# Performance work log

Measured on AMD Instinct MI355X. Metric: run time of the kernel, lower is better.

The kernel has to match this reference:

```python
import jax, jax.numpy as jnp
import numpy as np

DIM = 1024
HEADS = 16
HEAD_DIM = DIM // HEADS
EPS = 1e-5


def layer_norm(x, w, b):
    # normalize over last dim (head_dim)
    mu = jnp.mean(x, axis=-1, keepdims=True)
    var = jnp.mean(jnp.square(x - mu), axis=-1, keepdims=True)
    return (x - mu) * jax.lax.rsqrt(var + EPS) * w + b


def setup_inputs() -> dict:
    key = jax.random.key(0)
    ks = jax.random.split(key, 8)
    B, N = 2, 2048
    x = jax.random.normal(ks[0], (B, N, DIM), dtype=jnp.float32)
    mask = jax.random.randint(ks[1], (B, 1, N, N), 0, 2) == 1  # True = masked out
    qkv_w = jax.random.normal(ks[2], (3 * DIM, DIM), dtype=jnp.float32) * (DIM ** -0.5)
    q_norm_w = jnp.ones((HEAD_DIM,), dtype=jnp.float32)
    q_norm_b = jnp.zeros((HEAD_DIM,), dtype=jnp.float32)
    k_norm_w = jnp.ones((HEAD_DIM,), dtype=jnp.float32)
    k_norm_b = jnp.zeros((HEAD_DIM,), dtype=jnp.float32)
    proj_w = jax.random.normal(ks[3], (DIM, DIM), dtype=jnp.float32) * (DIM ** -0.5)
    proj_b = jnp.zeros((DIM,), dtype=jnp.float32)
    return {"x": x, "mask": mask, "qkv_w": qkv_w,
            "q_norm_w": q_norm_w, "q_norm_b": q_norm_b,
            "k_norm_w": k_norm_w, "k_norm_b": k_norm_b,
            "proj_w": proj_w, "proj_b": proj_b}


def reference(x, mask, qkv_w, q_norm_w, q_norm_b, k_norm_w, k_norm_b, proj_w, proj_b):
    B, N, C = x.shape
    H, D = HEADS, HEAD_DIM
    scale = D ** -0.5
    # qkv projection (no bias), split into q,k,v of shape (B,H,N,D)
    qkv = (x @ qkv_w.T).reshape(B, N, 3, H, D).transpose(2, 0, 3, 1, 4)
    q, k, v = qkv[0], qkv[1], qkv[2]
    q = layer_norm(q, q_norm_w, q_norm_b)
    k = layer_norm(k, k_norm_w, k_norm_b)
    q = q * scale
    attn = jnp.einsum("bhnd,bhmd->bhnm", q, k)  # (B,H,N,N)
    attn = jnp.where(mask, -jnp.inf, attn)
    attn = jax.nn.softmax(attn, axis=-1)
    out = jnp.einsum("bhnm,bhmd->bhnd", attn, v)
    out = out.transpose(0, 2, 1, 3).reshape(B, N, C)
    return out @ proj_w.T + proj_b
```

## Files before the change

kernel.cpp:

```cpp
#include <hip/hip_runtime.h>
#include <hip/hip_bf16.h>
#include <math.h>

#define B_    2
#define N_    2048
#define DIM_  1024
#define H_    16
#define HD_   64
#define EPS_  1e-5f
#define SCALE_ 0.125f
#define LOG2E_ 1.4426950408889634f
#define MFIX_  14.0f

typedef __attribute__((ext_vector_type(8))) __bf16 bf16x8;
typedef __attribute__((ext_vector_type(8))) unsigned short ushort8;
typedef __attribute__((ext_vector_type(4))) float f32x4;
typedef __attribute__((ext_vector_type(4))) unsigned int uint4v;

__device__ __forceinline__ unsigned short f2bf(float x) {
    unsigned u = __builtin_bit_cast(unsigned, x);
    u += 0x7fff + ((u >> 16) & 1);
    return (unsigned short)(u >> 16);
}
__device__ __forceinline__ unsigned pk2bf(float a, float b) {
    unsigned ua = __builtin_bit_cast(unsigned, a) + 0x8000u;
    unsigned ub = __builtin_bit_cast(unsigned, b) + 0x8000u;
    return __builtin_amdgcn_perm(ub, ua, 0x07060302);
}
__device__ __forceinline__ unsigned cvtpk(float a, float b) {
    unsigned r;
    asm("v_cvt_pk_bf16_f32 %0, %1, %2" : "=v"(r) : "v"(a), "v"(b));
    return r;
}

__device__ __forceinline__ void gl_lds16(const void* g, void* l) {
    __builtin_amdgcn_global_load_lds(
        (const __attribute__((address_space(1))) void*)g,
        (__attribute__((address_space(3))) void*)l, 16, 0, 0);
}

__global__ __launch_bounds__(256) void cast_all_bf16(
    const float* __restrict__ x, const float* __restrict__ qkvw,
    const float* __restrict__ pw, unsigned short* __restrict__ out) {
    int i = (blockIdx.x * 256 + threadIdx.x) * 8;
    const float* src;
    if (i < 4194304) src = x + i;
    else if (i < 7340032) src = qkvw + (i - 4194304);
    else src = pw + (i - 7340032);
    float4 v0 = *(const float4*)src;
    float4 v1 = *(const float4*)(src + 4);
    ushort8 r;
    r[0] = f2bf(v0.x); r[1] = f2bf(v0.y); r[2] = f2bf(v0.z); r[3] = f2bf(v0.w);
    r[4] = f2bf(v1.x); r[5] = f2bf(v1.y); r[6] = f2bf(v1.z); r[7] = f2bf(v1.w);
    *(ushort8*)(out + i) = r;
}

__global__ __launch_bounds__(256) void pack_mask(
    const int* __restrict__ mask, unsigned long long* __restrict__ bm) {
    int w = blockIdx.x * 4 + (threadIdx.x >> 6);
    int lane = threadIdx.x & 63;
    int mv = mask[(size_t)w * 64 + lane];
    unsigned long long bits = __ballot(mv != 0);
    if (lane == 0) bm[w] = bits;
}

__global__ __launch_bounds__(256) void gemm_qkv_ln(
    const unsigned short* __restrict__ A, const unsigned short* __restrict__ Bw,
    const float* __restrict__ qnw, const float* __restrict__ qnb,
    const float* __restrict__ knw, const float* __restrict__ knb,
    unsigned short* __restrict__ qbuf, unsigned short* __restrict__ kbuf,
    unsigned short* __restrict__ vt) {
    const int K = DIM_;
    __shared__ unsigned short As[128 * 32];
    __shared__ unsigned short Bs[128 * 32];
    const int tid = threadIdx.x;
    const int wave = tid >> 6, lane = tid & 63;
    const int quad = lane >> 4, lcol = lane & 15;
    const int wr = wave >> 1, wc = wave & 1;
    const int row0 = blockIdx.y * 128, col0 = blockIdx.x * 128;

    f32x4 acc[4][4];
#pragma unroll
    for (int i = 0; i < 4; ++i)
#pragma unroll
        for (int j = 0; j < 4; ++j) acc[i][j] = (f32x4){0.f, 0.f, 0.f, 0.f};

    for (int k0 = 0; k0 < K; k0 += 32) {
        __syncthreads();
#pragma unroll
        for (int c = 0; c < 2; ++c) {
            int base = wave * 2048 + c * 1024;
            int myofs = base + lane * 16;
            int r = myofs >> 6;
            int kb = myofs & 63;
            gl_lds16((const char*)A + ((size_t)(row0 + r) * K + k0) * 2 + kb,
                     (char*)As + base);
            gl_lds16((const char*)Bw + ((size_t)(col0 + r) * K + k0) * 2 + kb,
                     (char*)Bs + base);
        }
        __syncthreads();

        bf16x8 af[4], bfr[4];
#pragma unroll
        for (int i = 0; i < 4; ++i) {
            af[i] = *(const bf16x8*)&As[(wr * 64 + i * 16 + lcol) * 32 + quad * 8];
            bfr[i] = *(const bf16x8*)&Bs[(wc * 64 + i * 16 + lcol) * 32 + quad * 8];
        }
#pragma unroll
        for (int i = 0; i < 4; ++i)
#pragma unroll
            for (int j = 0; j < 4; ++j)
                acc[i][j] = __builtin_amdgcn_mfma_f32_16x16x32_bf16(
                    af[i], bfr[j], acc[i][j], 0, 0, 0);
    }

    const int colbase = col0 + wc * 64;
    const int t = colbase >> 10;
    const int h = (colbase & 1023) >> 6;

    if (t < 2) {
        const float* wv = (t == 0) ? qnw : knw;
        const float* bv = (t == 0) ? qnb : knb;
        float wreg[4], breg[4];
#pragma unroll
        for (int j = 0; j < 4; ++j) {
            wreg[j] = wv[j * 16 + lcol];
            breg[j] = bv[j * 16 + lcol];
        }
        const float sc = (t == 0) ? (SCALE_ * LOG2E_) : 1.f;
        unsigned short* obase = (t == 0) ? qbuf : kbuf;
#pragma unroll
        for (int i = 0; i < 4; ++i) {
#pragma unroll
            for (int reg = 0; reg < 4; ++reg) {
                int row = row0 + wr * 64 + i * 16 + quad * 4 + reg;
                int bb = row >> 11, n = row & (N_ - 1);
                float v[4];
#pragma unroll
                for (int j = 0; j < 4; ++j) v[j] = acc[i][j][reg];
                float s = v[0] + v[1] + v[2] + v[3];
                s += __shfl_xor(s, 1);
                s += __shfl_xor(s, 2);
                s += __shfl_xor(s, 4);
                s += __shfl_xor(s, 8);
                float mu = s * (1.f / 64.f);
                float d[4], s2 = 0.f;
#pragma unroll
                for (int j = 0; j < 4; ++j) {
                    d[j] = v[j] - mu;
                    s2 += d[j] * d[j];
                }
                s2 += __shfl_xor(s2, 1);
                s2 += __shfl_xor(s2, 2);
                s2 += __shfl_xor(s2, 4);
                s2 += __shfl_xor(s2, 8);
                float r = rsqrtf(s2 * (1.f / 64.f) + EPS_);
                float o0 = (d[0] * r * wreg[0] + breg[0]) * sc;
                float o1 = (d[1] * r * wreg[1] + breg[1]) * sc;
                float o2 = (d[2] * r * wreg[2] + breg[2]) * sc;
                float o3 = (d[3] * r * wreg[3] + breg[3]) * sc;
                uint2 pk;
                pk.x = pk2bf(o0, o1);
                pk.y = pk2bf(o2, o3);
                *(uint2*)(obase + ((size_t)(bb * H_ + h) * N_ + n) * 64 +
                          lcol * 4) = pk;
            }
        }
    } else {
        const int rowb = row0 + wr * 64;
        const int bb = rowb >> 11;
        unsigned short* vtb =
            vt + ((size_t)(bb * H_ + h) * 64) * (size_t)N_ + (rowb & (N_ - 1));
#pragma unroll
        for (int i = 0; i < 4; ++i) {
            const int pos = (i >> 1) * 32 + quad * 8 + (i & 1) * 4;
#pragma unroll
            for (int jj = 0; jj < 4; ++jj) {
                uint2 pk;
                pk.x = pk2bf(acc[i][jj][0], acc[i][jj][1]);
                pk.y = pk2bf(acc[i][jj][2], acc[i][jj][3]);
                *(uint2*)(vtb + (size_t)(lcol + 16 * jj) * N_ + pos) = pk;
            }
        }
    }
}

__global__ __launch_bounds__(256) void gemm_proj(
    const unsigned short* __restrict__ A, const unsigned short* __restrict__ Bw,
    const float* __restrict__ bias, float* __restrict__ Cout) {
    const int K = DIM_;
    __shared__ unsigned short As[128 * 32];
    __shared__ unsigned short Bs[64 * 32];
    const int tid = threadIdx.x;
    const int wave = tid >> 6, lane = tid & 63;
    const int quad = lane >> 4, lcol = lane & 15;
    const int row0 = blockIdx.y * 128, col0 = blockIdx.x * 64;

    f32x4 acc[2][4];
#pragma unroll
    for (int i = 0; i < 2; ++i)
#pragma unroll
        for (int j = 0; j < 4; ++j) acc[i][j] = (f32x4){0.f, 0.f, 0.f, 0.f};

    for (int k0 = 0; k0 < K; k0 += 32) {
        __syncthreads();
#pragma unroll
        for (int pi = 0; pi < 3; ++pi) {
            int p = wave * 3 + pi;
            if (p < 8) {
                int base = p * 1024;
                int myofs = base + lane * 16;
                int r = myofs >> 6, kb = myofs & 63;
                gl_lds16((const char*)A + ((size_t)(row0 + r) * K + k0) * 2 + kb,
                         (char*)As + base);
            } else {
                int base = (p - 8) * 1024;
                int myofs = base + lane * 16;
                int r = myofs >> 6, kb = myofs & 63;
                gl_lds16((const char*)Bw + ((size_t)(col0 + r) * K + k0) * 2 + kb,
                         (char*)Bs + base);
            }
        }
        __syncthreads();

        bf16x8 af[2], bfr[4];
#pragma unroll
        for (int i = 0; i < 2; ++i)
            af[i] = *(const bf16x8*)&As[(wave * 32 + i * 16 + lcol) * 32 + quad * 8];
#pragma unroll
        for (int j = 0; j < 4; ++j)
            bfr[j] = *(const bf16x8*)&Bs[(j * 16 + lcol) * 32 + quad * 8];
#pragma unroll
        for (int i = 0; i < 2; ++i)
#pragma unroll
            for (int j = 0; j < 4; ++j)
                acc[i][j] = __builtin_amdgcn_mfma_f32_16x16x32_bf16(
                    af[i], bfr[j], acc[i][j], 0, 0, 0);
    }

#pragma unroll
    for (int i = 0; i < 2; ++i) {
#pragma unroll
        for (int j = 0; j < 4; ++j) {
            int col = col0 + j * 16 + lcol;
            float bv = bias[col];
#pragma unroll
            for (int reg = 0; reg < 4; ++reg) {
                int row = row0 + wave * 32 + i * 16 + quad * 4 + reg;
                Cout[(size_t)row * DIM_ + col] = acc[i][j][reg] + bv;
            }
        }
    }
}

#define WAITBAR(Ncnt)                                                     \
    asm volatile("s_waitcnt vmcnt(" #Ncnt ")" ::: "memory");              \
    __builtin_amdgcn_s_barrier();                                         \
    __builtin_amdgcn_sched_barrier(0);

#define ISSUE2(B0, B1)                                                    \
    {                                                                     \
        gl_lds16(kp0, (char*)Ks[B0] + kld0);                              \
        gl_lds16(kp1, (char*)Ks[B0] + kld1);                              \
        gl_lds16(vp0, (char*)Vts[B0] + kld0);                             \
        gl_lds16(vp1, (char*)Vts[B0] + kld1);                             \
        gl_lds16(kp0 + 8192, (char*)Ks[B1] + kld0);                       \
        gl_lds16(kp1 + 8192, (char*)Ks[B1] + kld1);                       \
        gl_lds16(vp0 + 128, (char*)Vts[B1] + kld0);                       \
        gl_lds16(vp1 + 128, (char*)Vts[B1] + kld1);                       \
        mm0[B0] = bmq0[0]; mm1[B0] = bmq1[0];                             \
        mm0[B1] = bmq0[1]; mm1[B1] = bmq1[1];                             \
        kp0 += 16384; kp1 += 16384; vp0 += 256; vp1 += 256;               \
        bmq0 += 2; bmq1 += 2;                                             \
    }

#define QKT(J, SACC, MWA, MWB)                                            \
    {                                                                     \
        unsigned long long mqa = (MWA) >> (quad * 4);                     \
        unsigned long long mqb = (MWB) >> (quad * 4);                     \
        unsigned ml[2][2];                                                \
        ml[0][0] = (unsigned)mqa; ml[0][1] = (unsigned)(mqa >> 32);       \
        ml[1][0] = (unsigned)mqb; ml[1][1] = (unsigned)(mqb >> 32);       \
        _Pragma("unroll")                                                 \
        for (int qf = 0; qf < 2; ++qf)                                    \
            _Pragma("unroll")                                             \
            for (int kt = 0; kt < 4; ++kt) {                              \
                unsigned word = ml[qf][kt >> 1];                          \
                _Pragma("unroll")                                         \
                for (int reg = 0; reg < 4; ++reg) {                       \
                    unsigned msk = (unsigned)(((int)(word <<              \
                        (31 - ((kt & 1) * 16 + reg)))) >> 31);            \
                    SACC[qf][kt][reg] = __builtin_bit_cast(float,         \
                        (msk & 0xc61c4000u) | (~msk & 0xc1600000u));      \
                }                                                         \
            }                                                             \
        __builtin_amdgcn_s_setprio(1);                                    \
        _Pragma("unroll")                                                 \
        for (int kt = 0; kt < 4; ++kt)                                    \
            _Pragma("unroll")                                             \
            for (int d0 = 0; d0 < 2; ++d0) {                              \
                bf16x8 ak = *(const bf16x8*)((const char*)Ks[J] +         \
                    (d0 * 4 + quad) * 1024 + kt * 256 + lofs);            \
                SACC[0][kt] = __builtin_amdgcn_mfma_f32_16x16x32_bf16(    \
                    ak, bq[0][d0], SACC[0][kt], 0, 0, 0);                 \
                SACC[1][kt] = __builtin_amdgcn_mfma_f32_16x16x32_bf16(    \
                    ak, bq[1][d0], SACC[1][kt], 0, 0, 0);                 \
            }                                                             \
        __builtin_amdgcn_s_setprio(0);                                    \
    }

#define SM(SACC, PK)                                                      \
    _Pragma("unroll")                                                     \
    for (int qf = 0; qf < 2; ++qf)                                        \
        _Pragma("unroll")                                                 \
        for (int kt = 0; kt < 4; ++kt) {                                  \
            float p0 = exp2f(SACC[qf][kt][0]);                            \
            float p1 = exp2f(SACC[qf][kt][1]);                            \
            float p2 = exp2f(SACC[qf][kt][2]);                            \
            float p3 = exp2f(SACC[qf][kt][3]);                            \
            PK[qf][kt].x = cvtpk(p0, p1);                                 \
            PK[qf][kt].y = cvtpk(p2, p3);                                 \
        }

#define PV(J, PK)                                                         \
    {                                                                     \
        __builtin_amdgcn_s_setprio(1);                                    \
        _Pragma("unroll")                                                 \
        for (int P = 0; P < 2; ++P) {                                     \
            bf16x8 bp[2];                                                 \
            _Pragma("unroll")                                             \
            for (int qf = 0; qf < 2; ++qf) {                              \
                uint4v bu;                                                \
                bu[0] = PK[qf][2 * P].x;  bu[1] = PK[qf][2 * P].y;        \
                bu[2] = PK[qf][2 * P + 1].x; bu[3] = PK[qf][2 * P + 1].y; \
                bp[qf] = __builtin_bit_cast(bf16x8, bu);                  \
                lacc[qf] = __builtin_amdgcn_mfma_f32_16x16x32_bf16(       \
                    ones, bp[qf], lacc[qf], 0, 0, 0);                     \
            }                                                             \
            _Pragma("unroll")                                             \
            for (int dt = 0; dt < 4; ++dt) {                              \
                bf16x8 va = *(const bf16x8*)((const char*)Vts[J] +        \
                    (P * 4 + quad) * 1024 + dt * 256 + lofs);             \
                oacc[0][dt] = __builtin_amdgcn_mfma_f32_16x16x32_bf16(    \
                    va, bp[0], oacc[0][dt], 0, 0, 0);                     \
                oacc[1][dt] = __builtin_amdgcn_mfma_f32_16x16x32_bf16(    \
                    va, bp[1], oacc[1][dt], 0, 0, 0);                     \
            }                                                             \
        }                                                                 \
        __builtin_amdgcn_s_setprio(0);                                    \
    }

#define PAIR(J0, J1)                                                      \
    {                                                                     \
        f32x4 saccA[2][4], saccB[2][4];                                   \
        uint2 pkA[2][4], pkB[2][4];                                       \
        QKT(J0, saccA, mm0[J0], mm1[J0])                                  \
        SM(saccA, pkA)                                                    \
        QKT(J1, saccB, mm0[J1], mm1[J1])                                  \
        PV(J0, pkA)                                                       \
        SM(saccB, pkB)                                                    \
        PV(J1, pkB)                                                       \
    }

__global__ __launch_bounds__(256, 2) void flash_attn_mfma9(
    const unsigned short* __restrict__ q, const unsigned short* __restrict__ k,
    const unsigned short* __restrict__ vt,
    const unsigned long long* __restrict__ bm, unsigned short* __restrict__ ao) {
    __shared__ unsigned short Qs[128 * 64];
    __shared__ unsigned short Ks[4][64 * 64];
    __shared__ unsigned short Vts[4][64 * 64];

    const int tid = threadIdx.x;
    const int wave = tid >> 6, lane = tid & 63;
    const int quad = lane >> 4, lcol = lane & 15;
    const int bh = blockIdx.y, b = bh >> 4, h = bh & 15;
    const int q0 = blockIdx.x * 128;
    const int lofs = (lcol ^ (quad * 2)) << 4;

    const char* kgbase = (const char*)k + (size_t)bh * N_ * 128;
    const char* vtbase = (const char*)vt + (size_t)bh * 64 * N_ * 2;

    const int c0 = wave * 2, c1 = c0 + 1;
    const int swz0 = (c0 & 3) * 2, swz1 = (c1 & 3) * 2;
    const int kld0 = c0 * 1024, kld1 = c1 * 1024;
    const char* kp0 = kgbase + (lane ^ swz0) * 128 + c0 * 16;
    const char* kp1 = kgbase + (lane ^ swz1) * 128 + c1 * 16;
    const char* vp0 = vtbase + (size_t)(lane ^ swz0) * (N_ * 2) + c0 * 16;
    const char* vp1 = vtbase + (size_t)(lane ^ swz1) * (N_ * 2) + c1 * 16;

    const unsigned long long* bmq0 =
        bm + ((size_t)b * N_ + q0 + wave * 32 + lcol) * 32;
    const unsigned long long* bmq1 = bmq0 + 16 * 32;
    unsigned long long mm0[4], mm1[4];

    {
        const char* qg = (const char*)(q + (size_t)(bh * N_ + q0) * 64);
#pragma unroll
        for (int c = 0; c < 4; ++c) {
            int base = wave * 4096 + c * 1024;
            gl_lds16(qg + base + lane * 16, (char*)Qs + base);
        }
    }
    asm volatile("" ::: "memory");
    __builtin_amdgcn_sched_barrier(0);
#pragma unroll
    for (int t = 0; t < 4; ++t) {
        gl_lds16(kp0, (char*)Ks[t] + kld0);
        gl_lds16(kp1, (char*)Ks[t] + kld1);
        gl_lds16(vp0, (char*)Vts[t] + kld0);
        gl_lds16(vp1, (char*)Vts[t] + kld1);
        mm0[t] = bmq0[t];
        mm1[t] = bmq1[t];
        kp0 += 8192; kp1 += 8192; vp0 += 128; vp1 += 128;
        __builtin_amdgcn_sched_barrier(0);
    }
    bmq0 += 4; bmq1 += 4;
    asm volatile("s_waitcnt vmcnt(24)" ::: "memory");
    __builtin_amdgcn_sched_barrier(0);

    bf16x8 bq[2][2];
#pragma unroll
    for (int qf = 0; qf < 2; ++qf)
#pragma unroll
        for (int d0 = 0; d0 < 2; ++d0)
            bq[qf][d0] = *(const bf16x8*)&Qs[(wave * 32 + qf * 16 + lcol) * 64 +
                                             d0 * 32 + quad * 8];

    ushort8 ot;
#pragma unroll
    for (int i = 0; i < 8; ++i) ot[i] = 0x3F80;
    const bf16x8 ones = __builtin_bit_cast(bf16x8, ot);

    f32x4 oacc[2][4];
#pragma unroll
    for (int qf = 0; qf < 2; ++qf)
#pragma unroll
        for (int dt = 0; dt < 4; ++dt) oacc[qf][dt] = (f32x4){0.f, 0.f, 0.f, 0.f};
    f32x4 lacc[2];
    lacc[0] = (f32x4){0.f, 0.f, 0.f, 0.f};
    lacc[1] = (f32x4){0.f, 0.f, 0.f, 0.f};

    WAITBAR(12)
    PAIR(0, 1)
    for (int g = 0; g < 7; ++g) {
        WAITBAR(0)
        ISSUE2(0, 1)
        PAIR(2, 3)
        WAITBAR(0)
        ISSUE2(2, 3)
        PAIR(0, 1)
    }
    WAITBAR(0)
    PAIR(2, 3)

#pragma unroll
    for (int qf = 0; qf < 2; ++qf) {
        float inv = 1.f / lacc[qf][0];
        int row = q0 + wave * 32 + qf * 16 + lcol;
        unsigned short* dst =
            ao + ((size_t)(b * N_ + row)) * DIM_ + h * 64 + quad * 4;
#pragma unroll
        for (int dt = 0; dt < 4; ++dt) {
            uint2 pko;
            pko.x = pk2bf(oacc[qf][dt][0] * inv, oacc[qf][dt][1] * inv);
            pko.y = pk2bf(oacc[qf][dt][2] * inv, oacc[qf][dt][3] * inv);
            *(uint2*)(dst + dt * 16) = pko;
        }
    }
}

extern "C" void kernel_launch(void* const* d_in, const int* in_sizes, int n_in,
                              void* d_out, int out_size, void* d_ws,
                              size_t ws_size, hipStream_t stream) {
    const float* x     = (const float*)d_in[0];
    const int*   mask  = (const int*)d_in[1];
    const float* qkv_w = (const float*)d_in[2];
    const float* qnw   = (const float*)d_in[3];
    const float* qnb   = (const float*)d_in[4];
    const float* knw   = (const float*)d_in[5];
    const float* knb   = (const float*)d_in[6];
    const float* pw    = (const float*)d_in[7];
    const float* pb    = (const float*)d_in[8];
    float* out = (float*)d_out;

    char* ws = (char*)d_ws;
    unsigned short* x_bf  = (unsigned short*)(ws + 0);
    unsigned short* qw_bf = (unsigned short*)(ws + 8388608);
    unsigned short* pw_bf = (unsigned short*)(ws + 14680064);
    unsigned short* qbuf  = (unsigned short*)(ws + 16777216);
    unsigned short* kbuf  = (unsigned short*)(ws + 25165824);
    unsigned short* ao_bnc= (unsigned short*)(ws + 33554432);
    unsigned short* vt    = (unsigned short*)(ws + 41943040);
    unsigned long long* bmask = (unsigned long long*)(ws + 50331648);

    cast_all_bf16<<<8388608 / 2048, 256, 0, stream>>>(x, qkv_w, pw, x_bf);

    pack_mask<<<(B_ * N_ * (N_ / 64)) / 4, 256, 0, stream>>>(mask, bmask);

    gemm_qkv_ln<<<dim3(3072 / 128, 4096 / 128), 256, 0, stream>>>(
        x_bf, qw_bf, qnw, qnb, knw, knb, qbuf, kbuf, vt);

    flash_attn_mfma9<<<dim3(N_ / 128, B_ * H_), 256, 0, stream>>>(
        qbuf, kbuf, vt, bmask, ao_bnc);

    gemm_proj<<<dim3(DIM_ / 64, 4096 / 128), 256, 0, stream>>>(
        ao_bnc, pw_bf, pb, out);
}
```

Before: 267.6 us.

## Double query rows per wave in flash attention to reuse K/V tiles

Each wave now processes 64 query rows (four 16-row fragments) instead of 32, so the block covers 256 queries and the grid halves. Every K and V tile loaded into shared memory is reused across twice as many queries, which cuts global K/V traffic and LDS reads per MFMA. In exchange, register pressure roughly doubles for the accumulators, so launch bounds drop to one block per SM. The grid becomes 8x32=256 blocks, which lowers occupancy and may underfill the device's compute units.

```diff
diff --git a/kernel.cpp b/kernel.cpp
--- a/kernel.cpp
+++ b/kernel.cpp
@@ -268,24 +268,24 @@
         gl_lds16(kp1 + 8192, (char*)Ks[B1] + kld1);                       \
         gl_lds16(vp0 + 128, (char*)Vts[B1] + kld0);                       \
         gl_lds16(vp1 + 128, (char*)Vts[B1] + kld1);                       \
-        mm0[B0] = bmq0[0]; mm1[B0] = bmq1[0];                             \
-        mm0[B1] = bmq0[1]; mm1[B1] = bmq1[1];                             \
+        _Pragma("unroll")                                                 \
+        for (int qf = 0; qf < 4; ++qf) {                                  \
+            mm[B0][qf] = bmq[qf][0];                                      \
+            mm[B1][qf] = bmq[qf][1];                                      \
+            bmq[qf] += 2;                                                 \
+        }                                                                 \
         kp0 += 16384; kp1 += 16384; vp0 += 256; vp1 += 256;               \
-        bmq0 += 2; bmq1 += 2;                                             \
-    }
-
-#define QKT(J, SACC, MWA, MWB)                                            \
+    }
+
+#define QKT(J, SACC, MROW)                                                \
     {                                                                     \
-        unsigned long long mqa = (MWA) >> (quad * 4);                     \
-        unsigned long long mqb = (MWB) >> (quad * 4);                     \
-        unsigned ml[2][2];                                                \
-        ml[0][0] = (unsigned)mqa; ml[0][1] = (unsigned)(mqa >> 32);       \
-        ml[1][0] = (unsigned)mqb; ml[1][1] = (unsigned)(mqb >> 32);       \
         _Pragma("unroll")                                                 \
-        for (int qf = 0; qf < 2; ++qf)                                    \
+        for (int qf = 0; qf < 4; ++qf) {                                  \
+            unsigned long long mq = (MROW)[qf] >> (quad * 4);             \
+            unsigned mlo = (unsigned)mq, mhi = (unsigned)(mq >> 32);      \
             _Pragma("unroll")                                             \
             for (int kt = 0; kt < 4; ++kt) {                              \
-                unsigned word = ml[qf][kt >> 1];                          \
+                unsigned word = (kt < 2) ? mlo : mhi;                     \
                 _Pragma("unroll")                                         \
                 for (int reg = 0; reg < 4; ++reg) {                       \
                     unsigned msk = (unsigned)(((int)(word <<              \
@@ -294,6 +294,7 @@
                         (msk & 0xc61c4000u) | (~msk & 0xc1600000u));      \
                 }                                                         \
             }                                                             \
+        }                                                                 \
         __builtin_amdgcn_s_setprio(1);                                    \
         _Pragma("unroll")                                                 \
         for (int kt = 0; kt < 4; ++kt)                                    \
@@ -301,17 +302,17 @@
             for (int d0 = 0; d0 < 2; ++d0) {                              \
                 bf16x8 ak = *(const bf16x8*)((const char*)Ks[J] +         \
                     (d0 * 4 + quad) * 1024 + kt * 256 + lofs);            \
-                SACC[0][kt] = __builtin_amdgcn_mfma_f32_16x16x32_bf16(    \
-                    ak, bq[0][d0], SACC[0][kt], 0, 0, 0);                 \
-                SACC[1][kt] = __builtin_amdgcn_mfma_f32_16x16x32_bf16(    \
-                    ak, bq[1][d0], SACC[1][kt], 0, 0, 0);                 \
+                _Pragma("unroll")                                         \
+                for (int qf = 0; qf < 4; ++qf)                            \
+                    SACC[qf][kt] = __builtin_amdgcn_mfma_f32_16x16x32_bf16( \
+                        ak, bq[qf][d0], SACC[qf][kt], 0, 0, 0);           \
             }                                                             \
         __builtin_amdgcn_s_setprio(0);                                    \
     }
 
 #define SM(SACC, PK)                                                      \
     _Pragma("unroll")                                                     \
-    for (int qf = 0; qf < 2; ++qf)                                        \
+    for (int qf = 0; qf < 4; ++qf)                                        \
         _Pragma("unroll")                                                 \
         for (int kt = 0; kt < 4; ++kt) {                                  \
             float p0 = exp2f(SACC[qf][kt][0]);                            \
@@ -327,9 +328,9 @@
         __builtin_amdgcn_s_setprio(1);                                    \
         _Pragma("unroll")                                                 \
         for (int P = 0; P < 2; ++P) {                                     \
-            bf16x8 bp[2];                                                 \
+            bf16x8 bp[4];                                                 \
             _Pragma("unroll")                                             \
-            for (int qf = 0; qf < 2; ++qf) {                              \
+            for (int qf = 0; qf < 4; ++qf) {                              \
                 uint4v bu;                                                \
                 bu[0] = PK[qf][2 * P].x;  bu[1] = PK[qf][2 * P].y;        \
                 bu[2] = PK[qf][2 * P + 1].x; bu[3] = PK[qf][2 * P + 1].y; \
@@ -341,10 +342,10 @@
             for (int dt = 0; dt < 4; ++dt) {                              \
                 bf16x8 va = *(const bf16x8*)((const char*)Vts[J] +        \
                     (P * 4 + quad) * 1024 + dt * 256 + lofs);             \
-                oacc[0][dt] = __builtin_amdgcn_mfma_f32_16x16x32_bf16(    \
-                    va, bp[0], oacc[0][dt], 0, 0, 0);                     \
-                oacc[1][dt] = __builtin_amdgcn_mfma_f32_16x16x32_bf16(    \
-                    va, bp[1], oacc[1][dt], 0, 0, 0);                     \
+                _Pragma("unroll")                                         \
+                for (int qf = 0; qf < 4; ++qf)                            \
+                    oacc[qf][dt] = __builtin_amdgcn_mfma_f32_16x16x32_bf16( \
+                        va, bp[qf], oacc[qf][dt], 0, 0, 0);               \
             }                                                             \
         }                                                                 \
         __builtin_amdgcn_s_setprio(0);                                    \
@@ -352,21 +353,21 @@
 
 #define PAIR(J0, J1)                                                      \
     {                                                                     \
-        f32x4 saccA[2][4], saccB[2][4];                                   \
-        uint2 pkA[2][4], pkB[2][4];                                       \
-        QKT(J0, saccA, mm0[J0], mm1[J0])                                  \
+        f32x4 saccA[4][4], saccB[4][4];                                   \
+        uint2 pkA[4][4], pkB[4][4];                                       \
+        QKT(J0, saccA, mm[J0])                                            \
         SM(saccA, pkA)                                                    \
-        QKT(J1, saccB, mm0[J1], mm1[J1])                                  \
+        QKT(J1, saccB, mm[J1])                                            \
         PV(J0, pkA)                                                       \
         SM(saccB, pkB)                                                    \
         PV(J1, pkB)                                                       \
     }
 
-__global__ __launch_bounds__(256, 2) void flash_attn_mfma9(
+__global__ __launch_bounds__(256, 1) void flash_attn_mfma13(
     const unsigned short* __restrict__ q, const unsigned short* __restrict__ k,
     const unsigned short* __restrict__ vt,
     const unsigned long long* __restrict__ bm, unsigned short* __restrict__ ao) {
-    __shared__ unsigned short Qs[128 * 64];
+    __shared__ unsigned short Qs[256 * 64];
     __shared__ unsigned short Ks[4][64 * 64];
     __shared__ unsigned short Vts[4][64 * 64];
 
@@ -374,7 +375,7 @@
     const int wave = tid >> 6, lane = tid & 63;
     const int quad = lane >> 4, lcol = lane & 15;
     const int bh = blockIdx.y, b = bh >> 4, h = bh & 15;
-    const int q0 = blockIdx.x * 128;
+    const int q0 = blockIdx.x * 256;
     const int lofs = (lcol ^ (quad * 2)) << 4;
 
     const char* kgbase = (const char*)k + (size_t)bh * N_ * 128;
@@ -388,16 +389,17 @@
     const char* vp0 = vtbase + (size_t)(lane ^ swz0) * (N_ * 2) + c0 * 16;
     const char* vp1 = vtbase + (size_t)(lane ^ swz1) * (N_ * 2) + c1 * 16;
 
-    const unsigned long long* bmq0 =
-        bm + ((size_t)b * N_ + q0 + wave * 32 + lcol) * 32;
-    const unsigned long long* bmq1 = bmq0 + 16 * 32;
-    unsigned long long mm0[4], mm1[4];
+    const unsigned long long* bmq[4];
+#pragma unroll
+    for (int qf = 0; qf < 4; ++qf)
+        bmq[qf] = bm + ((size_t)b * N_ + q0 + wave * 64 + qf * 16 + lcol) * 32;
+    unsigned long long mm[4][4];
 
     {
         const char* qg = (const char*)(q + (size_t)(bh * N_ + q0) * 64);
 #pragma unroll
-        for (int c = 0; c < 4; ++c) {
-            int base = wave * 4096 + c * 1024;
+        for (int c = 0; c < 8; ++c) {
+            int base = wave * 8192 + c * 1024;
             gl_lds16(qg + base + lane * 16, (char*)Qs + base);
         }
     }
@@ -409,21 +411,22 @@
         gl_lds16(kp1, (char*)Ks[t] + kld1);
         gl_lds16(vp0, (char*)Vts[t] + kld0);
         gl_lds16(vp1, (char*)Vts[t] + kld1);
-        mm0[t] = bmq0[t];
-        mm1[t] = bmq1[t];
+#pragma unroll
+        for (int qf = 0; qf < 4; ++qf) mm[t][qf] = bmq[qf][t];
         kp0 += 8192; kp1 += 8192; vp0 += 128; vp1 += 128;
         __builtin_amdgcn_sched_barrier(0);
     }
-    bmq0 += 4; bmq1 += 4;
-    asm volatile("s_waitcnt vmcnt(24)" ::: "memory");
+#pragma unroll
+    for (int qf = 0; qf < 4; ++qf) bmq[qf] += 4;
+    asm volatile("s_waitcnt vmcnt(32)" ::: "memory");
     __builtin_amdgcn_sched_barrier(0);
 
-    bf16x8 bq[2][2];
-#pragma unroll
-    for (int qf = 0; qf < 2; ++qf)
+    bf16x8 bq[4][2];
+#pragma unroll
+    for (int qf = 0; qf < 4; ++qf)
 #pragma unroll
         for (int d0 = 0; d0 < 2; ++d0)
-            bq[qf][d0] = *(const bf16x8*)&Qs[(wave * 32 + qf * 16 + lcol) * 64 +
+            bq[qf][d0] = *(const bf16x8*)&Qs[(wave * 64 + qf * 16 + lcol) * 64 +
                                              d0 * 32 + quad * 8];
 
     ushort8 ot;
@@ -431,16 +434,16 @@
     for (int i = 0; i < 8; ++i) ot[i] = 0x3F80;
     const bf16x8 ones = __builtin_bit_cast(bf16x8, ot);
 
-    f32x4 oacc[2][4];
-#pragma unroll
-    for (int qf = 0; qf < 2; ++qf)
+    f32x4 oacc[4][4];
+#pragma unroll
+    for (int qf = 0; qf < 4; ++qf)
 #pragma unroll
         for (int dt = 0; dt < 4; ++dt) oacc[qf][dt] = (f32x4){0.f, 0.f, 0.f, 0.f};
-    f32x4 lacc[2];
-    lacc[0] = (f32x4){0.f, 0.f, 0.f, 0.f};
-    lacc[1] = (f32x4){0.f, 0.f, 0.f, 0.f};
-
-    WAITBAR(12)
+    f32x4 lacc[4];
+#pragma unroll
+    for (int qf = 0; qf < 4; ++qf) lacc[qf] = (f32x4){0.f, 0.f, 0.f, 0.f};
+
+    WAITBAR(16)
     PAIR(0, 1)
     for (int g = 0; g < 7; ++g) {
         WAITBAR(0)
@@ -454,9 +457,9 @@
     PAIR(2, 3)
 
 #pragma unroll
-    for (int qf = 0; qf < 2; ++qf) {
+    for (int qf = 0; qf < 4; ++qf) {
         float inv = 1.f / lacc[qf][0];
-        int row = q0 + wave * 32 + qf * 16 + lcol;
+        int row = q0 + wave * 64 + qf * 16 + lcol;
         unsigned short* dst =
             ao + ((size_t)(b * N_ + row)) * DIM_ + h * 64 + quad * 4;
 #pragma unroll
@@ -500,7 +503,7 @@
     gemm_qkv_ln<<<dim3(3072 / 128, 4096 / 128), 256, 0, stream>>>(
         x_bf, qw_bf, qnw, qnb, knw, knb, qbuf, kbuf, vt);
 
-    flash_attn_mfma9<<<dim3(N_ / 128, B_ * H_), 256, 0, stream>>>(
+    flash_attn_mfma13<<<dim3(N_ / 256, B_ * H_), 256, 0, stream>>>(
         qbuf, kbuf, vt, bmask, ao_bnc);
 
     gemm_proj<<<dim3(DIM_ / 64, 4096 / 128), 256, 0, stream>>>(
```

Measured after the change: 291.7 us. 9.0% more time.

## Double-buffer LDS in both GEMMs and merge cast/mask-pack kernels

Applied to the files above, without the earlier changes.

Both the QKV and projection GEMMs now use two LDS buffers, so the next K-slice is loaded with global_load_lds while MFMAs run on the current one. Each step has a single waitcnt+barrier in place of two __syncthreads, and MFMA sections are raised with s_setprio. The bf16 cast and mask bit-packing kernels are merged into one launch to save a kernel launch. The cost is double the LDS per block, which may lower occupancy.

```diff
diff --git a/kernel.cpp b/kernel.cpp
--- a/kernel.cpp
+++ b/kernel.cpp
@@ -39,30 +39,71 @@
         (__attribute__((address_space(3))) void*)l, 16, 0, 0);
 }
 
-__global__ __launch_bounds__(256) void cast_all_bf16(
+__global__ __launch_bounds__(256) void cast_and_pack(
     const float* __restrict__ x, const float* __restrict__ qkvw,
-    const float* __restrict__ pw, unsigned short* __restrict__ out) {
-    int i = (blockIdx.x * 256 + threadIdx.x) * 8;
-    const float* src;
-    if (i < 4194304) src = x + i;
-    else if (i < 7340032) src = qkvw + (i - 4194304);
-    else src = pw + (i - 7340032);
-    float4 v0 = *(const float4*)src;
-    float4 v1 = *(const float4*)(src + 4);
-    ushort8 r;
-    r[0] = f2bf(v0.x); r[1] = f2bf(v0.y); r[2] = f2bf(v0.z); r[3] = f2bf(v0.w);
-    r[4] = f2bf(v1.x); r[5] = f2bf(v1.y); r[6] = f2bf(v1.z); r[7] = f2bf(v1.w);
-    *(ushort8*)(out + i) = r;
-}
-
-__global__ __launch_bounds__(256) void pack_mask(
-    const int* __restrict__ mask, unsigned long long* __restrict__ bm) {
-    int w = blockIdx.x * 4 + (threadIdx.x >> 6);
-    int lane = threadIdx.x & 63;
-    int mv = mask[(size_t)w * 64 + lane];
-    unsigned long long bits = __ballot(mv != 0);
-    if (lane == 0) bm[w] = bits;
-}
+    const float* __restrict__ pw, const int* __restrict__ mask,
+    unsigned short* __restrict__ out, unsigned long long* __restrict__ bm) {
+    const int bid = blockIdx.x;
+    if (bid < 4096) {
+        int i = (bid * 256 + threadIdx.x) * 8;
+        const float* src;
+        if (i < 4194304) src = x + i;
+        else if (i < 7340032) src = qkvw + (i - 4194304);
+        else src = pw + (i - 7340032);
+        float4 v0 = *(const float4*)src;
+        float4 v1 = *(const float4*)(src + 4);
+        ushort8 r;
+        r[0] = f2bf(v0.x); r[1] = f2bf(v0.y); r[2] = f2bf(v0.z); r[3] = f2bf(v0.w);
+        r[4] = f2bf(v1.x); r[5] = f2bf(v1.y); r[6] = f2bf(v1.z); r[7] = f2bf(v1.w);
+        *(ushort8*)(out + i) = r;
+    } else {
+        int w = (bid - 4096) * 4 + (threadIdx.x >> 6);
+        int lane = threadIdx.x & 63;
+        int mv = mask[(size_t)w * 64 + lane];
+        unsigned long long bits = __ballot(mv != 0);
+        if (lane == 0) bm[w] = bits;
+    }
+}
+
+#define GWB                                                               \
+    asm volatile("s_waitcnt vmcnt(0)" ::: "memory");                      \
+    __builtin_amdgcn_s_barrier();                                         \
+    __builtin_amdgcn_sched_barrier(0);
+
+#define QSTAGE(BUF, K0)                                                   \
+    {                                                                     \
+        _Pragma("unroll")                                                 \
+        for (int c = 0; c < 2; ++c) {                                     \
+            int pbase = wave * 2048 + c * 1024;                           \
+            int myofs = pbase + lane * 16;                                \
+            int r = myofs >> 6;                                           \
+            int kb = myofs & 63;                                          \
+            gl_lds16((const char*)A + ((size_t)(row0 + r) * K + (K0)) * 2 + kb, \
+                     (char*)As[BUF] + pbase);                             \
+            gl_lds16((const char*)Bw + ((size_t)(col0 + r) * K + (K0)) * 2 + kb, \
+                     (char*)Bs[BUF] + pbase);                             \
+        }                                                                 \
+    }
+
+#define QCOMPUTE(BUF)                                                     \
+    {                                                                     \
+        bf16x8 af[4], bfr[4];                                             \
+        _Pragma("unroll")                                                 \
+        for (int i = 0; i < 4; ++i) {                                     \
+            af[i] = *(const bf16x8*)&As[BUF][(wr * 64 + i * 16 + lcol) * 32 + \
+                                            quad * 8];                    \
+            bfr[i] = *(const bf16x8*)&Bs[BUF][(wc * 64 + i * 16 + lcol) * 32 + \
+                                             quad * 8];                   \
+        }                                                                 \
+        __builtin_amdgcn_s_setprio(1);                                    \
+        _Pragma("unroll")                                                 \
+        for (int i = 0; i < 4; ++i)                                       \
+            _Pragma("unroll")                                             \
+            for (int j = 0; j < 4; ++j)                                   \
+                acc[i][j] = __builtin_amdgcn_mfma_f32_16x16x32_bf16(      \
+                    af[i], bfr[j], acc[i][j], 0, 0, 0);                   \
+        __builtin_amdgcn_s_setprio(0);                                    \
+    }
 
 __global__ __launch_bounds__(256) void gemm_qkv_ln(
     const unsigned short* __restrict__ A, const unsigned short* __restrict__ Bw,
@@ -71,8 +112,8 @@
     unsigned short* __restrict__ qbuf, unsigned short* __restrict__ kbuf,
     unsigned short* __restrict__ vt) {
     const int K = DIM_;
-    __shared__ unsigned short As[128 * 32];
-    __shared__ unsigned short Bs[128 * 32];
+    __shared__ unsigned short As[2][128 * 32];
+    __shared__ unsigned short Bs[2][128 * 32];
     const int tid = threadIdx.x;
     const int wave = tid >> 6, lane = tid & 63;
     const int quad = lane >> 4, lcol = lane & 15;
@@ -85,34 +126,20 @@
 #pragma unroll
         for (int j = 0; j < 4; ++j) acc[i][j] = (f32x4){0.f, 0.f, 0.f, 0.f};
 
-    for (int k0 = 0; k0 < K; k0 += 32) {
-        __syncthreads();
-#pragma unroll
-        for (int c = 0; c < 2; ++c) {
-            int base = wave * 2048 + c * 1024;
-            int myofs = base + lane * 16;
-            int r = myofs >> 6;
-            int kb = myofs & 63;
-            gl_lds16((const char*)A + ((size_t)(row0 + r) * K + k0) * 2 + kb,
-                     (char*)As + base);
-            gl_lds16((const char*)Bw + ((size_t)(col0 + r) * K + k0) * 2 + kb,
-                     (char*)Bs + base);
-        }
-        __syncthreads();
-
-        bf16x8 af[4], bfr[4];
-#pragma unroll
-        for (int i = 0; i < 4; ++i) {
-            af[i] = *(const bf16x8*)&As[(wr * 64 + i * 16 + lcol) * 32 + quad * 8];
-            bfr[i] = *(const bf16x8*)&Bs[(wc * 64 + i * 16 + lcol) * 32 + quad * 8];
-        }
-#pragma unroll
-        for (int i = 0; i < 4; ++i)
-#pragma unroll
-            for (int j = 0; j < 4; ++j)
-                acc[i][j] = __builtin_amdgcn_mfma_f32_16x16x32_bf16(
-                    af[i], bfr[j], acc[i][j], 0, 0, 0);
-    }
+    QSTAGE(0, 0)
+    GWB
+    for (int k0 = 0; k0 < K - 64; k0 += 64) {
+        QSTAGE(1, k0 + 32)
+        QCOMPUTE(0)
+        GWB
+        QSTAGE(0, k0 + 64)
+        QCOMPUTE(1)
+        GWB
+    }
+    QSTAGE(1, K - 32)
+    QCOMPUTE(0)
+    GWB
+    QCOMPUTE(1)
 
     const int colbase = col0 + wc * 64;
     const int t = colbase >> 10;
@@ -185,12 +212,55 @@
     }
 }
 
+#define PSTAGE(BUF, K0)                                                   \
+    {                                                                     \
+        _Pragma("unroll")                                                 \
+        for (int pi = 0; pi < 3; ++pi) {                                  \
+            int p = wave * 3 + pi;    \
+            if (p < 8) {                                                  \
+                int pbase = p * 1024;                                     \
+                int myofs = pbase + lane * 16;                            \
+                int r = myofs >> 6, kb = myofs & 63;                      \
+                gl_lds16((const char*)A +                                 \
+                             ((size_t)(row0 + r) * K + (K0)) * 2 + kb,    \
+                         (char*)As[BUF] + pbase);                         \
+            } else {                                                      \
+                int pbase = (p - 8) * 1024;                               \
+                int myofs = pbase + lane * 16;                            \
+                int r = myofs >> 6, kb = myofs & 63;                      \
+                gl_lds16((const char*)Bw +                                \
+                             ((size_t)(col0 + r) * K + (K0)) * 2 + kb,    \
+                         (char*)Bs[BUF] + pbase);                         \
+            }                                                             \
+        }                                                                 \
+    }
+
+#define PCOMPUTE(BUF)                                                     \
+    {                                                                     \
+        bf16x8 af[2], bfr[4];                                             \
+        _Pragma("unroll")                                                 \
+        for (int i = 0; i < 2; ++i)                                       \
+            af[i] = *(const bf16x8*)&As[BUF][(wave * 32 + i * 16 + lcol) * 32 + \
+                                            quad * 8];                    \
+        _Pragma("unroll")                                                 \
+        for (int j = 0; j < 4; ++j)                                       \
+            bfr[j] = *(const bf16x8*)&Bs[BUF][(j * 16 + lcol) * 32 + quad * 8]; \
+        __builtin_amdgcn_s_setprio(1);                                    \
+        _Pragma("unroll")                                                 \
+        for (int i = 0; i < 2; ++i)                                       \
+            _Pragma("unroll")                                             \
+            for (int j = 0; j < 4; ++j)                                   \
+                acc[i][j] = __builtin_amdgcn_mfma_f32_16x16x32_bf16(      \
+                    af[i], bfr[j], acc[i][j], 0, 0, 0);                   \
+        __builtin_amdgcn_s_setprio(0);                                    \
+    }
+
 __global__ __launch_bounds__(256) void gemm_proj(
     const unsigned short* __restrict__ A, const unsigned short* __restrict__ Bw,
     const float* __restrict__ bias, float* __restrict__ Cout) {
     const int K = DIM_;
-    __shared__ unsigned short As[128 * 32];
-    __shared__ unsigned short Bs[64 * 32];
+    __shared__ unsigned short As[2][128 * 32];
+    __shared__ unsigned short Bs[2][64 * 32];
     const int tid = threadIdx.x;
     const int wave = tid >> 6, lane = tid & 63;
     const int quad = lane >> 4, lcol = lane & 15;
@@ -202,41 +272,20 @@
 #pragma unroll
         for (int j = 0; j < 4; ++j) acc[i][j] = (f32x4){0.f, 0.f, 0.f, 0.f};
 
-    for (int k0 = 0; k0 < K; k0 += 32) {
-        __syncthreads();
-#pragma unroll
-        for (int pi = 0; pi < 3; ++pi) {
-            int p = wave * 3 + pi;
-            if (p < 8) {
-                int base = p * 1024;
-                int myofs = base + lane * 16;
-                int r = myofs >> 6, kb = myofs & 63;
-                gl_lds16((const char*)A + ((size_t)(row0 + r) * K + k0) * 2 + kb,
-                         (char*)As + base);
-            } else {
-                int base = (p - 8) * 1024;
-                int myofs = base + lane * 16;
-                int r = myofs >> 6, kb = myofs & 63;
-                gl_lds16((const char*)Bw + ((size_t)(col0 + r) * K + k0) * 2 + kb,
-                         (char*)Bs + base);
-            }
-        }
-        __syncthreads();
-
-        bf16x8 af[2], bfr[4];
-#pragma unroll
-        for (int i = 0; i < 2; ++i)
-            af[i] = *(const bf16x8*)&As[(wave * 32 + i * 16 + lcol) * 32 + quad * 8];
-#pragma unroll
-        for (int j = 0; j < 4; ++j)
-            bfr[j] = *(const bf16x8*)&Bs[(j * 16 + lcol) * 32 + quad * 8];
-#pragma unroll
-        for (int i = 0; i < 2; ++i)
-#pragma unroll
-            for (int j = 0; j < 4; ++j)
-                acc[i][j] = __builtin_amdgcn_mfma_f32_16x16x32_bf16(
-                    af[i], bfr[j], acc[i][j], 0, 0, 0);
-    }
+    PSTAGE(0, 0)
+    GWB
+    for (int k0 = 0; k0 < K - 64; k0 += 64) {
+        PSTAGE(1, k0 + 32)
+        PCOMPUTE(0)
+        GWB
+        PSTAGE(0, k0 + 64)
+        PCOMPUTE(1)
+        GWB
+    }
+    PSTAGE(1, K - 32)
+    PCOMPUTE(0)
+    GWB
+    PCOMPUTE(1)
 
 #pragma unroll
     for (int i = 0; i < 2; ++i) {
@@ -493,9 +542,8 @@
     unsigned short* vt    = (unsigned short*)(ws + 41943040);
     unsigned long long* bmask = (unsigned long long*)(ws + 50331648);
 
-    cast_all_bf16<<<8388608 / 2048, 256, 0, stream>>>(x, qkv_w, pw, x_bf);
-
-    pack_mask<<<(B_ * N_ * (N_ / 64)) / 4, 256, 0, stream>>>(mask, bmask);
+    cast_and_pack<<<4096 + 32768, 256, 0, stream>>>(
+        x, qkv_w, pw, mask, x_bf, bmask);
 
     gemm_qkv_ln<<<dim3(3072 / 128, 4096 / 128), 256, 0, stream>>>(
         x_bf, qw_bf, qnw, qnb, knw, knb, qbuf, kbuf, vt);
```

After: 247.8 us (median of 2 runs). 7.4% less time.
